# Kernel tuning notes

Measured on AMD Instinct MI355X. Metric: run time of the kernel, lower is better.

The kernel has to match this reference:

```python
import jax, jax.numpy as jnp
import numpy as np

EMBED_DIM = 256
N_HEADS = 8
N_LEVELS = 4
N_POINTS = 4
BATCH = 2
LEVEL_SHAPES = np.array([[64, 64], [32, 32], [16, 16], [8, 8]], dtype=np.int32)


def setup_inputs() -> dict:
    key = jax.random.key(0)
    ks = jax.random.split(key, 12)
    tok_per_img = int((LEVEL_SHAPES[:, 0] * LEVEL_SHAPES[:, 1]).sum())  # 5440
    n_q = BATCH * tok_per_img  # 10880
    level_spatial_shapes = jnp.asarray(LEVEL_SHAPES, jnp.int32)
    # queries are multi-level tokens, laid out level-by-level per image
    lvl = np.concatenate([np.full(int(h * w), l, np.int32) for l, (h, w) in enumerate(LEVEL_SHAPES)])
    query_level_indices = jnp.asarray(np.tile(lvl, BATCH), jnp.int32)
    query = jax.random.normal(ks[0], (n_q, EMBED_DIM), jnp.float32)
    pos01 = jax.random.uniform(ks[1], (n_q, 2), jnp.float32)
    query_spatial_positions = pos01 * level_spatial_shapes[query_level_indices].astype(jnp.float32)
    query_batch_offsets = jnp.asarray([i * tok_per_img for i in range(BATCH + 1)], jnp.int32)
    Hm, Wm = int(LEVEL_SHAPES[:, 0].max()), int(LEVEL_SHAPES[:, 1].max())
    feature_maps = jax.random.normal(ks[2], (BATCH, Hm, Wm, N_LEVELS, EMBED_DIM), jnp.float32)
    s = 0.02
    W_off = jax.random.normal(ks[3], (EMBED_DIM, N_POINTS * N_LEVELS * N_HEADS * 2), jnp.float32) * s
    b_off = jax.random.normal(ks[4], (N_POINTS * N_LEVELS * N_HEADS * 2,), jnp.float32)
    W_attn = jax.random.normal(ks[5], (EMBED_DIM, N_POINTS * N_LEVELS * N_HEADS), jnp.float32) * s
    b_attn = jnp.zeros((N_POINTS * N_LEVELS * N_HEADS,), jnp.float32)
    W_val = jax.random.normal(ks[6], (EMBED_DIM, EMBED_DIM), jnp.float32) * s
    b_val = jnp.zeros((EMBED_DIM,), jnp.float32)
    W_out = jax.random.normal(ks[7], (EMBED_DIM, EMBED_DIM), jnp.float32) * s
    b_out = jnp.zeros((EMBED_DIM,), jnp.float32)
    return {"query": query, "query_spatial_positions": query_spatial_positions,
            "query_batch_offsets": query_batch_offsets, "feature_maps": feature_maps,
            "level_spatial_shapes": level_spatial_shapes, "query_level_indices": query_level_indices,
            "W_off": W_off, "b_off": b_off, "W_attn": W_attn, "b_attn": b_attn,
            "W_val": W_val, "b_val": b_val, "W_out": W_out, "b_out": b_out}


def reference(query, query_spatial_positions, query_batch_offsets, feature_maps,
              level_spatial_shapes, query_level_indices,
              W_off, b_off, W_attn, b_attn, W_val, b_val, W_out, b_out):
    n_q = query.shape[0]
    B, Hm, Wm, L, D = feature_maps.shape
    H, P = N_HEADS, N_POINTS
    hd = D // H
    shapes_f = level_spatial_shapes.astype(query.dtype)  # [L,2]

    # Sparse tensor semantics: level l only has specified entries on its [H_l, W_l] grid;
    # value_proj is applied to specified values only, unspecified entries stay zero.
    hh = jnp.arange(Hm)[:, None, None]
    ww = jnp.arange(Wm)[None, :, None]
    valid = (hh < level_spatial_shapes[None, None, :, 0]) & (ww < level_spatial_shapes[None, None, :, 1])  # [Hm,Wm,L]
    values = (feature_maps @ W_val + b_val) * valid[None, :, :, :, None].astype(query.dtype)
    values = values.reshape(B, Hm, Wm, L, H, hd)  # split heads

    off = (query @ W_off + b_off).reshape(n_q, P, L, H, 2)
    attw = (query @ W_attn + b_attn).reshape(n_q, P * L, H)
    attw = jax.nn.softmax(attw, axis=-2).reshape(n_q, P, L, H)

    # rescale each query position to every level's coordinate system
    norm = query_spatial_positions / shapes_f[query_level_indices]  # [n_q,2]
    scaled = norm[:, None, :] * shapes_f  # [n_q,L,2]
    loc = scaled[:, None, :, None, :] + off  # [n_q,P,L,H,2]
    loc = jnp.clip(loc, 0.0, shapes_f[:, None, :])  # clamp to [0, level_shape]

    b_idx = jnp.searchsorted(query_batch_offsets, jnp.arange(n_q), side="right") - 1  # [n_q]

    h = loc[..., 0]
    w = loc[..., 1]
    h0 = jnp.floor(h)
    w0 = jnp.floor(w)
    fh = h - h0
    fw = w - w0
    h0i = h0.astype(jnp.int32)
    w0i = w0.astype(jnp.int32)

    Hl = level_spatial_shapes[None, None, :, None, 0]  # [1,1,L,1]
    Wl = level_spatial_shapes[None, None, :, None, 1]
    b_b = b_idx[:, None, None, None]
    l_b = jnp.arange(L)[None, None, :, None]
    head_b = jnp.arange(H)[None, None, None, :]

    def gather(hi, wi):
        # out-of-level-range lookups hit unspecified entries -> zero
        ok = (hi >= 0) & (hi < Hl) & (wi >= 0) & (wi < Wl)
        hi_c = jnp.clip(hi, 0, Hm - 1)
        wi_c = jnp.clip(wi, 0, Wm - 1)
        v = values[b_b, hi_c, wi_c, l_b, head_b]  # [n_q,P,L,H,hd]
        return v * ok[..., None].astype(v.dtype)

    sampled = (gather(h0i, w0i) * ((1 - fh) * (1 - fw))[..., None]
               + gather(h0i, w0i + 1) * ((1 - fh) * fw)[..., None]
               + gather(h0i + 1, w0i) * (fh * (1 - fw))[..., None]
               + gather(h0i + 1, w0i + 1) * (fh * fw)[..., None])  # [n_q,P,L,H,hd]

    out = jnp.einsum("qplhd,qplh->qhd", sampled, attw).reshape(n_q, D)
    return out @ W_out + b_out
```

## Files before the change

kernel.cpp:

```cpp
#include <hip/hip_runtime.h>
#include <math.h>

#define NQ   10880
#define TOK  5440

typedef short s16x8 __attribute__((ext_vector_type(8)));
typedef float f32x4 __attribute__((ext_vector_type(4)));

__device__ __forceinline__ float bf2f_lo(unsigned int u) {
    return __uint_as_float(u << 16);
}
__device__ __forceinline__ float bf2f_hi(unsigned int u) {
    return __uint_as_float(u & 0xFFFF0000u);
}
__device__ __forceinline__ unsigned short f2bf(float f) {
    unsigned int u = __float_as_uint(f);
    u += 0x7FFFu + ((u >> 16) & 1u);
    return (unsigned short)(u >> 16);
}
__device__ __forceinline__ unsigned int pack2(float a, float b) {
    return (unsigned int)f2bf(a) | ((unsigned int)f2bf(b) << 16);
}

__global__ __launch_bounds__(256) void prep_k(
    const float* __restrict__ query, const float* __restrict__ fm,
    const float* __restrict__ W_val, const float* __restrict__ W_off,
    const float* __restrict__ W_attn, const float* __restrict__ W_out,
    unsigned short* __restrict__ qbf, unsigned short* __restrict__ vsrc,
    unsigned short* __restrict__ WtAll)
{
    const int blk = blockIdx.x;
    const int tid = threadIdx.x;

    if (blk < 2720) {
        const int lin4 = blk * 256 + tid;
        float4 f = *(const float4*)(query + (size_t)lin4 * 4);
        uint2 o;
        o.x = pack2(f.x, f.y);
        o.y = pack2(f.z, f.w);
        *(uint2*)(qbf + (size_t)lin4 * 4) = o;
    } else if (blk < 5440) {
        const int lin4 = (blk - 2720) * 256 + tid;
        const int r = lin4 >> 6;
        const int c4 = (lin4 & 63) << 2;
        const int b = (r >= TOK) ? 1 : 0;
        const int t = r - b * TOK;
        int l, hh, ww;
        if (t < 4096)      { l = 0; hh = t >> 6; ww = t & 63; }
        else if (t < 5120) { int i = t - 4096; l = 1; hh = i >> 5; ww = i & 31; }
        else if (t < 5376) { int i = t - 5120; l = 2; hh = i >> 4; ww = i & 15; }
        else               { int i = t - 5376; l = 3; hh = i >> 3; ww = i & 7; }
        const float* p = fm + ((size_t)((((b * 64 + hh) * 64 + ww) * 4) + l) << 8) + c4;
        float4 f = *(const float4*)p;
        uint2 o;
        o.x = pack2(f.x, f.y);
        o.y = pack2(f.z, f.w);
        *(uint2*)(vsrc + (size_t)r * 256 + c4) = o;
    } else {
        __shared__ unsigned short T[64][72];
        const int bt = blk - 5440;
        const int kt = bt & 3;
        const int ct = bt >> 2;
        const int c0 = ct * 64;
        const float* Wp; int ldw, cl0;
        if (c0 < 256)      { Wp = W_val;  ldw = 256; cl0 = c0; }
        else if (c0 < 512) { Wp = W_off;  ldw = 256; cl0 = c0 - 256; }
        else if (c0 < 640) { Wp = W_attn; ldw = 128; cl0 = c0 - 512; }
        else               { Wp = W_out;  ldw = 256; cl0 = c0 - 640; }

        const int kk = tid >> 2;
        const int cq = (tid & 3) << 4;
        const float* src = Wp + (size_t)(kt * 64 + kk) * ldw + cl0 + cq;
        float4 f0 = *(const float4*)(src);
        float4 f1 = *(const float4*)(src + 4);
        float4 f2 = *(const float4*)(src + 8);
        float4 f3 = *(const float4*)(src + 12);
        uint4 w0, w1;
        w0.x = pack2(f0.x, f0.y); w0.y = pack2(f0.z, f0.w);
        w0.z = pack2(f1.x, f1.y); w0.w = pack2(f1.z, f1.w);
        w1.x = pack2(f2.x, f2.y); w1.y = pack2(f2.z, f2.w);
        w1.z = pack2(f3.x, f3.y); w1.w = pack2(f3.z, f3.w);
        *(uint4*)&T[kk][cq]     = w0;
        *(uint4*)&T[kk][cq + 8] = w1;
        __syncthreads();
        const int cc = tid >> 2;
        const int kq = (tid & 3) << 4;
        union { unsigned short u[16]; uint4 q[2]; } ob;
#pragma unroll
        for (int j = 0; j < 16; ++j) ob.u[j] = T[kq + j][cc];
        unsigned short* dst = WtAll + (size_t)(c0 + cc) * 256 + kt * 64 + kq;
        *(uint4*)(dst)     = ob.q[0];
        *(uint4*)(dst + 8) = ob.q[1];
    }
}

__global__ __launch_bounds__(256) void gemm_bf16_k(
    const unsigned short* __restrict__ A1, const unsigned short* __restrict__ A2,
    const unsigned short* __restrict__ Wt,
    const float* __restrict__ bias1, const float* __restrict__ bias2,
    const float* __restrict__ bias3,
    void* __restrict__ C1, void* __restrict__ C2, int mode)
{
    __shared__ unsigned short As[128][72];
    __shared__ unsigned short Bs[128][72];

    const int tid = threadIdx.x;
    const int bm = blockIdx.x, bn = blockIdx.y;

    const unsigned short* A;
    const float* bias;
    void* Cp; int ldc, col0, cbf, wr0;
    if (mode == 0) {
        if (bn < 2) {
            A = A1; wr0 = bn * 128; bias = bias1 + bn * 128;
            Cp = C1; ldc = 256; col0 = bn * 128; cbf = 1;
        } else {
            A = A2; wr0 = bn * 128;
            bias = (bn < 4) ? bias2 + (bn - 2) * 128 : bias3;
            Cp = C2; ldc = 384; col0 = (bn - 2) * 128; cbf = 0;
        }
    } else {
        A = A1; wr0 = 640 + bn * 128; bias = bias1 + bn * 128;
        Cp = C1; ldc = 256; col0 = bn * 128; cbf = 0;
    }

    const int sr  = tid >> 1;
    const int skc = (tid & 1) << 5;
    const unsigned short* Ap = A  + (size_t)(bm * 128 + sr) * 256 + skc;
    const unsigned short* Bp = Wt + (size_t)(wr0 + sr) * 256 + skc;

    const int w = tid >> 6, lane = tid & 63;
    const int quad = lane >> 4, fl = lane & 15;
    const int quad8 = quad << 3;
    const int mW = (w >> 1) << 6, nW = (w & 1) << 6;

    f32x4 acc[4][4] = {};

    for (int k0 = 0; k0 < 256; k0 += 64) {
        uint4 av0 = *(const uint4*)(Ap + k0);
        uint4 av1 = *(const uint4*)(Ap + k0 + 8);
        uint4 av2 = *(const uint4*)(Ap + k0 + 16);
        uint4 av3 = *(const uint4*)(Ap + k0 + 24);
        uint4 bv0 = *(const uint4*)(Bp + k0);
        uint4 bv1 = *(const uint4*)(Bp + k0 + 8);
        uint4 bv2 = *(const uint4*)(Bp + k0 + 16);
        uint4 bv3 = *(const uint4*)(Bp + k0 + 24);
        __syncthreads();
        *(uint4*)&As[sr][skc]      = av0;
        *(uint4*)&As[sr][skc + 8]  = av1;
        *(uint4*)&As[sr][skc + 16] = av2;
        *(uint4*)&As[sr][skc + 24] = av3;
        *(uint4*)&Bs[sr][skc]      = bv0;
        *(uint4*)&Bs[sr][skc + 8]  = bv1;
        *(uint4*)&Bs[sr][skc + 16] = bv2;
        *(uint4*)&Bs[sr][skc + 24] = bv3;
        __syncthreads();
#pragma unroll
        for (int ks = 0; ks < 64; ks += 32) {
            s16x8 af[4], bf[4];
#pragma unroll
            for (int i = 0; i < 4; ++i) {
                af[i] = *(const s16x8*)&As[mW + i * 16 + fl][ks + quad8];
                bf[i] = *(const s16x8*)&Bs[nW + i * 16 + fl][ks + quad8];
            }
#pragma unroll
            for (int i = 0; i < 4; ++i)
#pragma unroll
                for (int j = 0; j < 4; ++j)
                    acc[i][j] = __builtin_amdgcn_mfma_f32_16x16x32_bf16(
                        af[i], bf[j], acc[i][j], 0, 0, 0);
        }
    }

    float* Cf = (float*)Cp;
    unsigned short* Cb = (unsigned short*)Cp;
#pragma unroll
    for (int j = 0; j < 4; ++j) {
        const int c = nW + j * 16 + fl;
        const float bv = bias[c];
        const int cg = col0 + c;
#pragma unroll
        for (int i = 0; i < 4; ++i) {
            const int row0 = bm * 128 + mW + i * 16 + (quad << 2);
#pragma unroll
            for (int r = 0; r < 4; ++r) {
                const float v = acc[i][j][r] + bv;
                if (cbf) Cb[(size_t)(row0 + r) * ldc + cg] = f2bf(v);
                else     Cf[(size_t)(row0 + r) * ldc + cg] = v;
            }
        }
    }
}

__global__ __launch_bounds__(256) void sample_k(
    const float* __restrict__ offattn,
    const unsigned short* __restrict__ values,
    const float* __restrict__ qpos,
    const int*   __restrict__ qlevel,
    unsigned short* __restrict__ qout)
{
    __shared__ float  sRow[8][384];
    __shared__ float4 sW[8][128];
    __shared__ int4   sIdx[8][128];

    const int tid = threadIdx.x;

    const int band = blockIdx.x & 7;
    const int g    = blockIdx.x >> 3;
    const int bat  = g / 85;
    const int i0   = (g % 85) << 3;
    int qs;
    if (i0 < 512)      qs = band * 512 + i0;
    else if (i0 < 640) qs = 4096 + band * 128 + (i0 - 512);
    else if (i0 < 672) qs = 5120 + band * 32 + (i0 - 640);
    else               qs = 5376 + band * 8;
    const int qbase = bat * TOK + qs;

    {
        const float4* rb = (const float4*)(offattn + (size_t)qbase * 384);
        float4* sf = (float4*)sRow;
#pragma unroll
        for (int i = 0; i < 3; ++i) sf[tid + i * 256] = rb[tid + i * 256];
    }
    __syncthreads();

    if (tid < 64) {
        const int qn = tid >> 3, h = tid & 7;
        float m = -1e30f;
#pragma unroll
        for (int j = 0; j < 16; ++j) m = fmaxf(m, sRow[qn][256 + j * 8 + h]);
        float e[16], s = 0.f;
#pragma unroll
        for (int j = 0; j < 16; ++j) { e[j] = __expf(sRow[qn][256 + j * 8 + h] - m); s += e[j]; }
        float inv = 1.0f / s;
#pragma unroll
        for (int j = 0; j < 16; ++j) sRow[qn][256 + j * 8 + h] = e[j] * inv;
    }
    __syncthreads();

    const int LBASE[4] = {0, 4096, 5120, 5376};
#pragma unroll
    for (int ss = 0; ss < 4; ++ss) {
        const int s  = tid + ss * 256;
        const int qn = s >> 7;
        const int c  = s & 127;
        const int pl = c >> 3;
        const int l  = pl & 3;
        const int q  = qbase + qn;
        const int b  = (q >= TOK) ? 1 : 0;
        const float ph = qpos[2 * q], pw = qpos[2 * q + 1];
        const int ql = qlevel[q];
        const float invq = 1.0f / (float)(64 >> ql);
        const int Hl = 64 >> l;
        const float Hlf = (float)Hl;
        const float sc = invq * Hlf;
        float lh = ph * sc + sRow[qn][2 * c];
        float lw = pw * sc + sRow[qn][2 * c + 1];
        const float aw = sRow[qn][256 + c];
        lh = fminf(fmaxf(lh, 0.f), Hlf);
        lw = fminf(fmaxf(lw, 0.f), Hlf);
        const float fh0 = floorf(lh), fw0 = floorf(lw);
        const int h0 = (int)fh0, w0 = (int)fw0;
        const float fh = lh - fh0, fw = lw - fw0;
        float w00 = (1.f - fh) * (1.f - fw);
        float w01 = (1.f - fh) * fw;
        float w10 = fh * (1.f - fw);
        float w11 = fh * fw;
        if (h0     >= Hl) { w00 = 0.f; w01 = 0.f; }
        if (h0 + 1 >= Hl) { w10 = 0.f; w11 = 0.f; }
        if (w0     >= Hl) { w00 = 0.f; w10 = 0.f; }
        if (w0 + 1 >= Hl) { w01 = 0.f; w11 = 0.f; }
        const int h0c = min(h0, Hl - 1), h1c = min(h0 + 1, Hl - 1);
        const int w0c = min(w0, Hl - 1), w1c = min(w0 + 1, Hl - 1);
        const int base = b * TOK + LBASE[l];
        sW[qn][c]   = make_float4(aw * w00, aw * w01, aw * w10, aw * w11);
        sIdx[qn][c] = make_int4((base + h0c * Hl + w0c) << 8,
                                (base + h0c * Hl + w1c) << 8,
                                (base + h1c * Hl + w0c) << 8,
                                (base + h1c * Hl + w1c) << 8);
    }
    __syncthreads();

    const int qn = tid >> 5;
    const int t  = tid & 31;
    const int h  = t >> 2;
    const int dg = t & 3;
    const unsigned short* vb = values + h * 32 + (dg << 3);
    float a[8] = {};
#pragma unroll
    for (int pl = 0; pl < 16; ++pl) {
        const int c = pl * 8 + h;
        const float4 wt = sW[qn][c];
        const int4  id = sIdx[qn][c];
        const uint4 u00 = *(const uint4*)(vb + id.x);
        const uint4 u01 = *(const uint4*)(vb + id.y);
        const uint4 u10 = *(const uint4*)(vb + id.z);
        const uint4 u11 = *(const uint4*)(vb + id.w);
#define ACC8(U, W)                                         \
        a[0] = fmaf(W, bf2f_lo(U.x), a[0]);                \
        a[1] = fmaf(W, bf2f_hi(U.x), a[1]);                \
        a[2] = fmaf(W, bf2f_lo(U.y), a[2]);                \
        a[3] = fmaf(W, bf2f_hi(U.y), a[3]);                \
        a[4] = fmaf(W, bf2f_lo(U.z), a[4]);                \
        a[5] = fmaf(W, bf2f_hi(U.z), a[5]);                \
        a[6] = fmaf(W, bf2f_lo(U.w), a[6]);                \
        a[7] = fmaf(W, bf2f_hi(U.w), a[7]);
        ACC8(u00, wt.x)
        ACC8(u01, wt.y)
        ACC8(u10, wt.z)
        ACC8(u11, wt.w)
#undef ACC8
    }
    const int q = qbase + qn;
    uint4 o;
    o.x = pack2(a[0], a[1]);
    o.y = pack2(a[2], a[3]);
    o.z = pack2(a[4], a[5]);
    o.w = pack2(a[6], a[7]);
    *(uint4*)(qout + (size_t)q * 256 + h * 32 + (dg << 3)) = o;
}

extern "C" void kernel_launch(void* const* d_in, const int* in_sizes, int n_in,
                              void* d_out, int out_size, void* d_ws, size_t ws_size,
                              hipStream_t stream)
{
    const float* query  = (const float*)d_in[0];
    const float* qpos   = (const float*)d_in[1];
    const float* fm     = (const float*)d_in[3];
    const int*   qlvl   = (const int*)d_in[5];
    const float* W_off  = (const float*)d_in[6];
    const float* b_off  = (const float*)d_in[7];
    const float* W_attn = (const float*)d_in[8];
    const float* b_attn = (const float*)d_in[9];
    const float* W_val  = (const float*)d_in[10];
    const float* b_val  = (const float*)d_in[11];
    const float* W_out  = (const float*)d_in[12];
    const float* b_out  = (const float*)d_in[13];
    float* out = (float*)d_out;

    char* ws = (char*)d_ws;
    unsigned short* vsrc    = (unsigned short*)ws;
    unsigned short* qbf     = vsrc + (size_t)NQ * 256;
    unsigned short* WtAll   = qbf + (size_t)NQ * 256;
    unsigned short* values  = WtAll + (size_t)896 * 256;
    unsigned short* qout    = values + (size_t)NQ * 256;
    float*          offattn = (float*)(qout + (size_t)NQ * 256);

    dim3 blk(256);
    prep_k<<<dim3(5496), blk, 0, stream>>>(query, fm, W_val, W_off, W_attn, W_out,
                                           qbf, vsrc, WtAll);
    gemm_bf16_k<<<dim3(85, 5), blk, 0, stream>>>(vsrc, qbf, WtAll,
                                                 b_val, b_off, b_attn,
                                                 values, offattn, 0);
    sample_k<<<dim3(NQ / 8), blk, 0, stream>>>(offattn, values, qpos, qlvl, qout);
    gemm_bf16_k<<<dim3(85, 2), blk, 0, stream>>>(qout, nullptr, WtAll,
                                                 b_out, nullptr, nullptr,
                                                 out, nullptr, 1);
}
```

Measured before the change: 156.3 us.

## Fuse fp32-to-bf16 activation conversion into GEMM A-tile loads

Removes the separate conversion of query and feature maps to bf16 buffers and instead converts fp32 data to bf16 while loading A tiles inside the GEMM, including the level-gather addressing for feature maps. The prep kernel now only transposes weights. This drops a full write and reread of two intermediate activation buffers and simplifies the launch, at the cost of wider fp32 global loads and conversion ALU work repeated across the column blocks that share each row tile.

```diff
diff --git a/kernel.cpp b/kernel.cpp
--- a/kernel.cpp
+++ b/kernel.cpp
@@ -22,27 +22,85 @@
     return (unsigned int)f2bf(a) | ((unsigned int)f2bf(b) << 16);
 }
 
-__global__ __launch_bounds__(256) void prep_k(
-    const float* __restrict__ query, const float* __restrict__ fm,
+__global__ __launch_bounds__(256) void prepW_k(
     const float* __restrict__ W_val, const float* __restrict__ W_off,
     const float* __restrict__ W_attn, const float* __restrict__ W_out,
-    unsigned short* __restrict__ qbf, unsigned short* __restrict__ vsrc,
     unsigned short* __restrict__ WtAll)
 {
-    const int blk = blockIdx.x;
+    __shared__ unsigned short T[64][72];
+    const int bt = blockIdx.x;
     const int tid = threadIdx.x;
-
-    if (blk < 2720) {
-        const int lin4 = blk * 256 + tid;
-        float4 f = *(const float4*)(query + (size_t)lin4 * 4);
-        uint2 o;
-        o.x = pack2(f.x, f.y);
-        o.y = pack2(f.z, f.w);
-        *(uint2*)(qbf + (size_t)lin4 * 4) = o;
-    } else if (blk < 5440) {
-        const int lin4 = (blk - 2720) * 256 + tid;
-        const int r = lin4 >> 6;
-        const int c4 = (lin4 & 63) << 2;
+    const int kt = bt & 3;
+    const int ct = bt >> 2;
+    const int c0 = ct * 64;
+    const float* Wp; int ldw, cl0;
+    if (c0 < 256)      { Wp = W_val;  ldw = 256; cl0 = c0; }
+    else if (c0 < 512) { Wp = W_off;  ldw = 256; cl0 = c0 - 256; }
+    else if (c0 < 640) { Wp = W_attn; ldw = 128; cl0 = c0 - 512; }
+    else               { Wp = W_out;  ldw = 256; cl0 = c0 - 640; }
+
+    const int kk = tid >> 2;
+    const int cq = (tid & 3) << 4;
+    const float* src = Wp + (size_t)(kt * 64 + kk) * ldw + cl0 + cq;
+    float4 f0 = *(const float4*)(src);
+    float4 f1 = *(const float4*)(src + 4);
+    float4 f2 = *(const float4*)(src + 8);
+    float4 f3 = *(const float4*)(src + 12);
+    uint4 w0, w1;
+    w0.x = pack2(f0.x, f0.y); w0.y = pack2(f0.z, f0.w);
+    w0.z = pack2(f1.x, f1.y); w0.w = pack2(f1.z, f1.w);
+    w1.x = pack2(f2.x, f2.y); w1.y = pack2(f2.z, f2.w);
+    w1.z = pack2(f3.x, f3.y); w1.w = pack2(f3.z, f3.w);
+    *(uint4*)&T[kk][cq]     = w0;
+    *(uint4*)&T[kk][cq + 8] = w1;
+    __syncthreads();
+    const int cc = tid >> 2;
+    const int kq = (tid & 3) << 4;
+    union { unsigned short u[16]; uint4 q[2]; } ob;
+#pragma unroll
+    for (int j = 0; j < 16; ++j) ob.u[j] = T[kq + j][cc];
+    unsigned short* dst = WtAll + (size_t)(c0 + cc) * 256 + kt * 64 + kq;
+    *(uint4*)(dst)     = ob.q[0];
+    *(uint4*)(dst + 8) = ob.q[1];
+}
+
+__global__ __launch_bounds__(256) void gemm_fused_k(
+    const float* __restrict__ query, const float* __restrict__ fm,
+    const unsigned short* __restrict__ qoutbf,
+    const unsigned short* __restrict__ Wt,
+    const float* __restrict__ b_val, const float* __restrict__ b_off,
+    const float* __restrict__ b_attn, const float* __restrict__ b_out,
+    unsigned short* __restrict__ values, float* __restrict__ offattn,
+    float* __restrict__ out, int mode)
+{
+    __shared__ unsigned short As[128][72];
+    __shared__ unsigned short Bs[128][72];
+
+    const int tid = threadIdx.x;
+    const int bm = blockIdx.x, bn = blockIdx.y;
+
+    const float* bias;
+    void* Cp; int ldc, col0, cbf, wr0;
+    if (mode == 0) {
+        if (bn < 2) {
+            wr0 = bn * 128; bias = b_val + bn * 128;
+            Cp = values; ldc = 256; col0 = bn * 128; cbf = 1;
+        } else {
+            wr0 = bn * 128;
+            bias = (bn < 4) ? b_off + (bn - 2) * 128 : b_attn;
+            Cp = offattn; ldc = 384; col0 = (bn - 2) * 128; cbf = 0;
+        }
+    } else {
+        wr0 = 640 + bn * 128; bias = b_out + bn * 128;
+        Cp = out; ldc = 256; col0 = bn * 128; cbf = 0;
+    }
+
+    const int asrc = (mode == 1) ? 2 : ((bn < 2) ? 0 : 1);
+    const int r   = bm * 128 + (tid >> 1);
+    const int skc = (tid & 1) << 5;
+    const float* a32 = nullptr;
+    const unsigned short* a16 = nullptr;
+    if (asrc == 0) {
         const int b = (r >= TOK) ? 1 : 0;
         const int t = r - b * TOK;
         int l, hh, ww;
@@ -50,83 +108,14 @@
         else if (t < 5120) { int i = t - 4096; l = 1; hh = i >> 5; ww = i & 31; }
         else if (t < 5376) { int i = t - 5120; l = 2; hh = i >> 4; ww = i & 15; }
         else               { int i = t - 5376; l = 3; hh = i >> 3; ww = i & 7; }
-        const float* p = fm + ((size_t)((((b * 64 + hh) * 64 + ww) * 4) + l) << 8) + c4;
-        float4 f = *(const float4*)p;
-        uint2 o;
-        o.x = pack2(f.x, f.y);
-        o.y = pack2(f.z, f.w);
-        *(uint2*)(vsrc + (size_t)r * 256 + c4) = o;
+        a32 = fm + ((size_t)((((b * 64 + hh) * 64 + ww) * 4) + l) << 8) + skc;
+    } else if (asrc == 1) {
+        a32 = query + (size_t)r * 256 + skc;
     } else {
-        __shared__ unsigned short T[64][72];
-        const int bt = blk - 5440;
-        const int kt = bt & 3;
-        const int ct = bt >> 2;
-        const int c0 = ct * 64;
-        const float* Wp; int ldw, cl0;
-        if (c0 < 256)      { Wp = W_val;  ldw = 256; cl0 = c0; }
-        else if (c0 < 512) { Wp = W_off;  ldw = 256; cl0 = c0 - 256; }
-        else if (c0 < 640) { Wp = W_attn; ldw = 128; cl0 = c0 - 512; }
-        else               { Wp = W_out;  ldw = 256; cl0 = c0 - 640; }
-
-        const int kk = tid >> 2;
-        const int cq = (tid & 3) << 4;
-        const float* src = Wp + (size_t)(kt * 64 + kk) * ldw + cl0 + cq;
-        float4 f0 = *(const float4*)(src);
-        float4 f1 = *(const float4*)(src + 4);
-        float4 f2 = *(const float4*)(src + 8);
-        float4 f3 = *(const float4*)(src + 12);
-        uint4 w0, w1;
-        w0.x = pack2(f0.x, f0.y); w0.y = pack2(f0.z, f0.w);
-        w0.z = pack2(f1.x, f1.y); w0.w = pack2(f1.z, f1.w);
-        w1.x = pack2(f2.x, f2.y); w1.y = pack2(f2.z, f2.w);
-        w1.z = pack2(f3.x, f3.y); w1.w = pack2(f3.z, f3.w);
-        *(uint4*)&T[kk][cq]     = w0;
-        *(uint4*)&T[kk][cq + 8] = w1;
-        __syncthreads();
-        const int cc = tid >> 2;
-        const int kq = (tid & 3) << 4;
-        union { unsigned short u[16]; uint4 q[2]; } ob;
-#pragma unroll
-        for (int j = 0; j < 16; ++j) ob.u[j] = T[kq + j][cc];
-        unsigned short* dst = WtAll + (size_t)(c0 + cc) * 256 + kt * 64 + kq;
-        *(uint4*)(dst)     = ob.q[0];
-        *(uint4*)(dst + 8) = ob.q[1];
-    }
-}
-
-__global__ __launch_bounds__(256) void gemm_bf16_k(
-    const unsigned short* __restrict__ A1, const unsigned short* __restrict__ A2,
-    const unsigned short* __restrict__ Wt,
-    const float* __restrict__ bias1, const float* __restrict__ bias2,
-    const float* __restrict__ bias3,
-    void* __restrict__ C1, void* __restrict__ C2, int mode)
-{
-    __shared__ unsigned short As[128][72];
-    __shared__ unsigned short Bs[128][72];
-
-    const int tid = threadIdx.x;
-    const int bm = blockIdx.x, bn = blockIdx.y;
-
-    const unsigned short* A;
-    const float* bias;
-    void* Cp; int ldc, col0, cbf, wr0;
-    if (mode == 0) {
-        if (bn < 2) {
-            A = A1; wr0 = bn * 128; bias = bias1 + bn * 128;
-            Cp = C1; ldc = 256; col0 = bn * 128; cbf = 1;
-        } else {
-            A = A2; wr0 = bn * 128;
-            bias = (bn < 4) ? bias2 + (bn - 2) * 128 : bias3;
-            Cp = C2; ldc = 384; col0 = (bn - 2) * 128; cbf = 0;
-        }
-    } else {
-        A = A1; wr0 = 640 + bn * 128; bias = bias1 + bn * 128;
-        Cp = C1; ldc = 256; col0 = bn * 128; cbf = 0;
-    }
-
-    const int sr  = tid >> 1;
-    const int skc = (tid & 1) << 5;
-    const unsigned short* Ap = A  + (size_t)(bm * 128 + sr) * 256 + skc;
+        a16 = qoutbf + (size_t)r * 256 + skc;
+    }
+
+    const int sr = tid >> 1;
     const unsigned short* Bp = Wt + (size_t)(wr0 + sr) * 256 + skc;
 
     const int w = tid >> 6, lane = tid & 63;
@@ -137,19 +126,40 @@
     f32x4 acc[4][4] = {};
 
     for (int k0 = 0; k0 < 256; k0 += 64) {
-        uint4 av0 = *(const uint4*)(Ap + k0);
-        uint4 av1 = *(const uint4*)(Ap + k0 + 8);
-        uint4 av2 = *(const uint4*)(Ap + k0 + 16);
-        uint4 av3 = *(const uint4*)(Ap + k0 + 24);
+        uint4 av[4];
+        if (a16) {
+            av[0] = *(const uint4*)(a16 + k0);
+            av[1] = *(const uint4*)(a16 + k0 + 8);
+            av[2] = *(const uint4*)(a16 + k0 + 16);
+            av[3] = *(const uint4*)(a16 + k0 + 24);
+        } else {
+            const float* s = a32 + k0;
+            float4 f0 = *(const float4*)(s);
+            float4 f1 = *(const float4*)(s + 4);
+            float4 f2 = *(const float4*)(s + 8);
+            float4 f3 = *(const float4*)(s + 12);
+            float4 f4 = *(const float4*)(s + 16);
+            float4 f5 = *(const float4*)(s + 20);
+            float4 f6 = *(const float4*)(s + 24);
+            float4 f7 = *(const float4*)(s + 28);
+            av[0].x = pack2(f0.x, f0.y); av[0].y = pack2(f0.z, f0.w);
+            av[0].z = pack2(f1.x, f1.y); av[0].w = pack2(f1.z, f1.w);
+            av[1].x = pack2(f2.x, f2.y); av[1].y = pack2(f2.z, f2.w);
+            av[1].z = pack2(f3.x, f3.y); av[1].w = pack2(f3.z, f3.w);
+            av[2].x = pack2(f4.x, f4.y); av[2].y = pack2(f4.z, f4.w);
+            av[2].z = pack2(f5.x, f5.y); av[2].w = pack2(f5.z, f5.w);
+            av[3].x = pack2(f6.x, f6.y); av[3].y = pack2(f6.z, f6.w);
+            av[3].z = pack2(f7.x, f7.y); av[3].w = pack2(f7.z, f7.w);
+        }
         uint4 bv0 = *(const uint4*)(Bp + k0);
         uint4 bv1 = *(const uint4*)(Bp + k0 + 8);
         uint4 bv2 = *(const uint4*)(Bp + k0 + 16);
         uint4 bv3 = *(const uint4*)(Bp + k0 + 24);
         __syncthreads();
-        *(uint4*)&As[sr][skc]      = av0;
-        *(uint4*)&As[sr][skc + 8]  = av1;
-        *(uint4*)&As[sr][skc + 16] = av2;
-        *(uint4*)&As[sr][skc + 24] = av3;
+        *(uint4*)&As[sr][skc]      = av[0];
+        *(uint4*)&As[sr][skc + 8]  = av[1];
+        *(uint4*)&As[sr][skc + 16] = av[2];
+        *(uint4*)&As[sr][skc + 24] = av[3];
         *(uint4*)&Bs[sr][skc]      = bv0;
         *(uint4*)&Bs[sr][skc + 8]  = bv1;
         *(uint4*)&Bs[sr][skc + 16] = bv2;
@@ -183,10 +193,10 @@
         for (int i = 0; i < 4; ++i) {
             const int row0 = bm * 128 + mW + i * 16 + (quad << 2);
 #pragma unroll
-            for (int r = 0; r < 4; ++r) {
-                const float v = acc[i][j][r] + bv;
-                if (cbf) Cb[(size_t)(row0 + r) * ldc + cg] = f2bf(v);
-                else     Cf[(size_t)(row0 + r) * ldc + cg] = v;
+            for (int rr = 0; rr < 4; ++rr) {
+                const float v = acc[i][j][rr] + bv;
+                if (cbf) Cb[(size_t)(row0 + rr) * ldc + cg] = f2bf(v);
+                else     Cf[(size_t)(row0 + rr) * ldc + cg] = v;
             }
         }
     }
@@ -339,21 +349,18 @@
     float* out = (float*)d_out;
 
     char* ws = (char*)d_ws;
-    unsigned short* vsrc    = (unsigned short*)ws;
-    unsigned short* qbf     = vsrc + (size_t)NQ * 256;
-    unsigned short* WtAll   = qbf + (size_t)NQ * 256;
+    unsigned short* WtAll   = (unsigned short*)ws;
     unsigned short* values  = WtAll + (size_t)896 * 256;
     unsigned short* qout    = values + (size_t)NQ * 256;
     float*          offattn = (float*)(qout + (size_t)NQ * 256);
 
     dim3 blk(256);
-    prep_k<<<dim3(5496), blk, 0, stream>>>(query, fm, W_val, W_off, W_attn, W_out,
-                                           qbf, vsrc, WtAll);
-    gemm_bf16_k<<<dim3(85, 5), blk, 0, stream>>>(vsrc, qbf, WtAll,
-                                                 b_val, b_off, b_attn,
-                                                 values, offattn, 0);
+    prepW_k<<<dim3(56), blk, 0, stream>>>(W_val, W_off, W_attn, W_out, WtAll);
+    gemm_fused_k<<<dim3(85, 5), blk, 0, stream>>>(query, fm, nullptr, WtAll,
+                                                  b_val, b_off, b_attn, b_out,
+                                                  values, offattn, out, 0);
     sample_k<<<dim3(NQ / 8), blk, 0, stream>>>(offattn, values, qpos, qlvl, qout);
-    gemm_bf16_k<<<dim3(85, 2), blk, 0, stream>>>(qout, nullptr, WtAll,
-                                                 b_out, nullptr, nullptr,
-                                                 out, nullptr, 1);
-}
+    gemm_fused_k<<<dim3(85, 2), blk, 0, stream>>>(query, fm, qout, WtAll,
+                                                  b_val, b_off, b_attn, b_out,
+                                                  values, offattn, out, 1);
+}
```

Result: slower. 161.2 us (+3.1%).
